# Kernel tuning notes

Measured on AMD Instinct MI355X. Metric: run time of the kernel, lower is better.

## Reference

```python
import jax, jax.numpy as jnp
import numpy as np

N_NODES = 100000

def _gcn_conv(x, W, b, src, dst, ew, num_nodes):
    # x: [N, Fin], W: [Fin, Fout], src/dst: [Etot], ew: [Etot]
    xw = x @ W                                   # [N, Fout]
    deg = jax.ops.segment_sum(ew, dst, num_segments=num_nodes)   # [N]
    dinv = jnp.where(deg > 0, jax.lax.rsqrt(jnp.where(deg > 0, deg, 1.0)), 0.0)
    norm = dinv[src] * ew * dinv[dst]            # [Etot]
    msg = xw[src] * norm[:, None]                # [Etot, Fout] gather-transform
    out = jax.ops.segment_sum(msg, dst, num_segments=num_nodes)  # scatter-add
    return out + b

def setup_inputs() -> dict:
    key = jax.random.key(0)
    k1, k2, k3, k4, k5, k6, k7 = jax.random.split(key, 7)
    N, E, F_IN, HID, CLS = N_NODES, 1600000, 128, 64, 32
    x = jax.random.normal(k1, (N, F_IN), dtype=jnp.float32)
    edge_index = jax.random.randint(k2, (2, E), 0, N, dtype=jnp.int64)
    edge_weight = jax.random.uniform(k3, (E,), dtype=jnp.float32)
    s1 = 1.0 / np.sqrt(F_IN)
    s2 = 1.0 / np.sqrt(HID)
    W1 = jax.random.uniform(k4, (F_IN, HID), dtype=jnp.float32, minval=-s1, maxval=s1)
    b1 = jnp.zeros((HID,), dtype=jnp.float32)
    W2 = jax.random.uniform(k5, (HID, CLS), dtype=jnp.float32, minval=-s2, maxval=s2)
    b2 = jnp.zeros((CLS,), dtype=jnp.float32)
    return {"x": x, "edge_index": edge_index, "edge_weight": edge_weight,
            "W1": W1, "b1": b1, "W2": W2, "b2": b2}

def reference(x, edge_index, edge_weight, W1, b1, W2, b2):
    N = x.shape[0]
    # add self-loops with weight 1 (PyG GCNConv default)
    loop = jnp.arange(N, dtype=edge_index.dtype)
    src = jnp.concatenate([edge_index[0], loop])
    dst = jnp.concatenate([edge_index[1], loop])
    ew = jnp.concatenate([edge_weight, jnp.ones((N,), dtype=edge_weight.dtype)])
    h = _gcn_conv(x, W1, b1, src, dst, ew, N)
    h = jax.nn.relu(h)
    # dropout is identity in eval mode
    out = _gcn_conv(h, W2, b2, src, dst, ew, N)
    return out
```

## Files before the change

### kernel.cpp

```cpp
#include <hip/hip_runtime.h>

#define FIN 128
#define HID 64
#define CLS 32

#define BSH 7
#define BNODES 128
#define GB 256
#define BCAP 4096

__device__ inline unsigned short f2bf(float x) {
  unsigned u = __float_as_uint(x);
  return (unsigned short)((u + 0x7FFFu + ((u >> 16) & 1u)) >> 16);
}
__device__ inline void bf8_to_f32(int4 v, float* f) {
  f[0] = __uint_as_float((unsigned)v.x << 16);
  f[1] = __uint_as_float((unsigned)v.x & 0xFFFF0000u);
  f[2] = __uint_as_float((unsigned)v.y << 16);
  f[3] = __uint_as_float((unsigned)v.y & 0xFFFF0000u);
  f[4] = __uint_as_float((unsigned)v.z << 16);
  f[5] = __uint_as_float((unsigned)v.z & 0xFFFF0000u);
  f[6] = __uint_as_float((unsigned)v.w << 16);
  f[7] = __uint_as_float((unsigned)v.w & 0xFFFF0000u);
}

__global__ __launch_bounds__(256) void k_a1(const int* __restrict__ dst,
                                            int* __restrict__ gcntT,
                                            int E, int CHUNK, int NBUK) {
  __shared__ int cnt[1024];
  for (int i = threadIdx.x; i < NBUK; i += 256) cnt[i] = 0;
  __syncthreads();
  int s = blockIdx.x * CHUNK, e = min(E, s + CHUNK);
  for (int p = s + threadIdx.x; p < e; p += 256)
    atomicAdd(&cnt[dst[p] >> BSH], 1);
  __syncthreads();
  for (int i = threadIdx.x; i < NBUK; i += 256)
    gcntT[i * GB + blockIdx.x] = cnt[i];
}

__global__ __launch_bounds__(256) void k_scan_sums(const int* __restrict__ counts,
                                                   int* __restrict__ bsum, int N) {
  __shared__ int s[256];
  int base = blockIdx.x * 1024 + threadIdx.x * 4;
  int t = 0;
#pragma unroll
  for (int j = 0; j < 4; ++j)
    if (base + j < N) t += counts[base + j];
  s[threadIdx.x] = t;
  __syncthreads();
  for (int off = 128; off > 0; off >>= 1) {
    if (threadIdx.x < off) s[threadIdx.x] += s[threadIdx.x + off];
    __syncthreads();
  }
  if (threadIdx.x == 0) bsum[blockIdx.x] = s[0];
}

__global__ __launch_bounds__(256) void k_scan_bsums(int* __restrict__ bsum, int nb) {
  __shared__ int s[256];
  int t = threadIdx.x;
  int v = (t < nb) ? bsum[t] : 0;
  s[t] = v;
  __syncthreads();
  for (int off = 1; off < 256; off <<= 1) {
    int u = (t >= off) ? s[t - off] : 0;
    __syncthreads();
    s[t] += u;
    __syncthreads();
  }
  if (t < nb) bsum[t] = s[t] - v;
}

__global__ __launch_bounds__(256) void k_scan_emit(const int* __restrict__ counts,
                                                   const int* __restrict__ bsum,
                                                   int* __restrict__ rowstart, int N) {
  __shared__ int s[256];
  int base = blockIdx.x * 1024 + threadIdx.x * 4;
  int c[4];
#pragma unroll
  for (int j = 0; j < 4; ++j) c[j] = (base + j < N) ? counts[base + j] : 0;
  int tsum = c[0] + c[1] + c[2] + c[3];
  s[threadIdx.x] = tsum;
  __syncthreads();
  for (int off = 1; off < 256; off <<= 1) {
    int v = (threadIdx.x >= off) ? s[threadIdx.x - off] : 0;
    __syncthreads();
    s[threadIdx.x] += v;
    __syncthreads();
  }
  int run = bsum[blockIdx.x] + s[threadIdx.x] - tsum;
#pragma unroll
  for (int j = 0; j < 4; ++j) {
    if (base + j < N) rowstart[base + j] = run;
    run += c[j];
  }
}

__global__ __launch_bounds__(256) void k_a2(const int* __restrict__ src,
                                            const int* __restrict__ dst,
                                            const float* __restrict__ ew,
                                            const int* __restrict__ goff,
                                            int2* __restrict__ recs,
                                            int E, int CHUNK, int NBUK) {
  __shared__ int cur[1024];
  for (int i = threadIdx.x; i < NBUK; i += 256)
    cur[i] = goff[i * GB + blockIdx.x];
  __syncthreads();
  int s = blockIdx.x * CHUNK, e = min(E, s + CHUNK);
  for (int p = s + threadIdx.x; p < e; p += 256) {
    int d = dst[p];
    int b = d >> BSH;
    int pos = atomicAdd(&cur[b], 1);
    recs[pos] = make_int2(src[p] | ((d & (BNODES - 1)) << 17), __float_as_int(ew[p]));
  }
}

__global__ __launch_bounds__(256) void k_bucket(int2* __restrict__ recs,
                                                const int* __restrict__ goff,
                                                float* __restrict__ dinv,
                                                int* __restrict__ rowstart,
                                                int N, int E, int NBUK) {
  __shared__ int2 lrec[BCAP];
  __shared__ int cnt[BNODES];
  __shared__ int cur[BNODES];
  __shared__ int sbuf[BNODES];
  __shared__ float degs[BNODES];
  __shared__ float dl[BNODES];
  const int b = blockIdx.x;
  const int t = threadIdx.x;
  const int bstart = goff[b * GB];
  const int bend = (b + 1 < NBUK) ? goff[(b + 1) * GB] : E;
  int m = bend - bstart;
  if (m > BCAP) m = BCAP;

  if (t < BNODES) { cnt[t] = 0; degs[t] = 1.0f; }
  __syncthreads();
  for (int p = t; p < m; p += 256) {
    int2 r = recs[bstart + p];
    lrec[p] = r;
    int d = (r.x >> 17) & (BNODES - 1);
    atomicAdd(&cnt[d], 1);
    atomicAdd(&degs[d], __int_as_float(r.y));
  }
  __syncthreads();
  if (t < BNODES) sbuf[t] = cnt[t];
  __syncthreads();
  for (int off = 1; off < BNODES; off <<= 1) {
    int v = (t < BNODES && t >= off) ? sbuf[t - off] : 0;
    __syncthreads();
    if (t < BNODES) sbuf[t] += v;
    __syncthreads();
  }
  if (t < BNODES) {
    int ls = sbuf[t] - cnt[t];
    cur[t] = ls;
    float di = rsqrtf(degs[t]);
    dl[t] = di;
    int node = b * BNODES + t;
    if (node < N) { dinv[node] = di; rowstart[node] = bstart + ls; }
  }
  __syncthreads();
  for (int p = t; p < m; p += 256) {
    int2 r = lrec[p];
    int d = (r.x >> 17) & (BNODES - 1);
    int pos = atomicAdd(&cur[d], 1);
    float c = __int_as_float(r.y) * dl[d];
    recs[bstart + pos] = make_int2(r.x & 0x1FFFF, __float_as_int(c));
  }
}

template <int K, int F, bool RELU, int BLK, int R, int MINW>
__global__ __launch_bounds__(BLK, MINW) void gemm_kernel(const float* __restrict__ x,
                                                         const float* __restrict__ w,
                                                         const float* __restrict__ scale,
                                                         unsigned short* __restrict__ y, int N) {
  constexpr int CG = F / 4;
  constexpr int RG = BLK / CG;
  constexpr int ROWS = RG * R;
  __shared__ float sW[K * F];
  for (int i = threadIdx.x * 4; i < K * F; i += BLK * 4)
    *(float4*)&sW[i] = *(const float4*)&w[i];
  __syncthreads();

  const int tx = threadIdx.x % CG;
  const int ty = threadIdx.x / CG;
  const int row0 = blockIdx.x * ROWS + ty * R;
  const int col0 = tx * 4;
  if (row0 >= N) return;

  const float* xr[R];
#pragma unroll
  for (int r = 0; r < R; ++r) {
    int rr = (row0 + r < N) ? (row0 + r) : (N - 1);
    xr[r] = x + (size_t)rr * K;
  }

  float acc[R][4] = {{0.f}};
  float4 xv[R], nx[R];
#pragma unroll
  for (int r = 0; r < R; ++r) xv[r] = *(const float4*)&xr[r][0];

  auto step = [&](int k) {
    float4 w0 = *(const float4*)&sW[(k + 0) * F + col0];
    float4 w1 = *(const float4*)&sW[(k + 1) * F + col0];
    float4 w2 = *(const float4*)&sW[(k + 2) * F + col0];
    float4 w3 = *(const float4*)&sW[(k + 3) * F + col0];
#pragma unroll
    for (int r = 0; r < R; ++r) {
      float4 xc = xv[r];
      if (RELU) {
        xc.x = fmaxf(xc.x, 0.f); xc.y = fmaxf(xc.y, 0.f);
        xc.z = fmaxf(xc.z, 0.f); xc.w = fmaxf(xc.w, 0.f);
      }
      acc[r][0] += xc.x * w0.x + xc.y * w1.x + xc.z * w2.x + xc.w * w3.x;
      acc[r][1] += xc.x * w0.y + xc.y * w1.y + xc.z * w2.y + xc.w * w3.y;
      acc[r][2] += xc.x * w0.z + xc.y * w1.z + xc.z * w2.z + xc.w * w3.z;
      acc[r][3] += xc.x * w0.w + xc.y * w1.w + xc.z * w2.w + xc.w * w3.w;
    }
  };

#pragma unroll 4
  for (int k = 0; k < K - 4; k += 4) {
#pragma unroll
    for (int r = 0; r < R; ++r) nx[r] = *(const float4*)&xr[r][k + 4];
    step(k);
#pragma unroll
    for (int r = 0; r < R; ++r) xv[r] = nx[r];
  }
  step(K - 4);

#pragma unroll
  for (int r = 0; r < R; ++r)
    if (row0 + r < N) {
      float sc = scale[row0 + r];
      ushort4 o;
      o.x = f2bf(sc * acc[r][0]); o.y = f2bf(sc * acc[r][1]);
      o.z = f2bf(sc * acc[r][2]); o.w = f2bf(sc * acc[r][3]);
      *(ushort4*)&y[(size_t)(row0 + r) * F + col0] = o;
    }
}

template <int F>
__global__ __launch_bounds__(256) void pull_agg(const unsigned short* __restrict__ xs,
                                                const int2* __restrict__ pairs,
                                                const int* __restrict__ rowstart,
                                                const float* __restrict__ dinv,
                                                const float* __restrict__ b,
                                                float* __restrict__ out, int N, int E) {
  constexpr int LPN = F / 8;
  constexpr int NPB = 256 / LPN;
  const int g = blockIdx.x * NPB + threadIdx.x / LPN;
  const int f8 = (threadIdx.x % LPN) * 8;
  if (g >= N) return;

  const int start = rowstart[g];
  const int end = (g + 1 < N) ? rowstart[g + 1] : E;
  const float di = dinv[g];

  float acc[8];
  {
    int4 v = *(const int4*)&xs[(size_t)g * F + f8];
    float xf[8];
    bf8_to_f32(v, xf);
    float4 b0 = *(const float4*)&b[f8];
    float4 b1 = *(const float4*)&b[f8 + 4];
    acc[0] = fmaf(di, xf[0], b0.x); acc[1] = fmaf(di, xf[1], b0.y);
    acc[2] = fmaf(di, xf[2], b0.z); acc[3] = fmaf(di, xf[3], b0.w);
    acc[4] = fmaf(di, xf[4], b1.x); acc[5] = fmaf(di, xf[5], b1.y);
    acc[6] = fmaf(di, xf[6], b1.z); acc[7] = fmaf(di, xf[7], b1.w);
  }

  int p = start;
  for (; p + 2 <= end; p += 2) {
    int2 p0 = pairs[p];
    int2 p1 = pairs[p + 1];
    int4 v0 = *(const int4*)&xs[(size_t)p0.x * F + f8];
    int4 v1 = *(const int4*)&xs[(size_t)p1.x * F + f8];
    float c0 = __int_as_float(p0.y), c1 = __int_as_float(p1.y);
    float x0[8], x1[8];
    bf8_to_f32(v0, x0);
    bf8_to_f32(v1, x1);
#pragma unroll
    for (int j = 0; j < 8; ++j) acc[j] = fmaf(c0, x0[j], acc[j]);
#pragma unroll
    for (int j = 0; j < 8; ++j) acc[j] = fmaf(c1, x1[j], acc[j]);
  }
  if (p < end) {
    int2 pa = pairs[p];
    int4 va = *(const int4*)&xs[(size_t)pa.x * F + f8];
    float ca = __int_as_float(pa.y);
    float xa[8];
    bf8_to_f32(va, xa);
#pragma unroll
    for (int j = 0; j < 8; ++j) acc[j] = fmaf(ca, xa[j], acc[j]);
  }
  *(float4*)&out[(size_t)g * F + f8] = make_float4(acc[0], acc[1], acc[2], acc[3]);
  *(float4*)&out[(size_t)g * F + f8 + 4] = make_float4(acc[4], acc[5], acc[6], acc[7]);
}

extern "C" void kernel_launch(void* const* d_in, const int* in_sizes, int n_in,
                              void* d_out, int out_size, void* d_ws, size_t ws_size,
                              hipStream_t stream) {
  const float* x  = (const float*)d_in[0];
  const int*   ei = (const int*)d_in[1];
  const float* ew = (const float*)d_in[2];
  const float* W1 = (const float*)d_in[3];
  const float* b1 = (const float*)d_in[4];
  const float* W2 = (const float*)d_in[5];
  const float* b2 = (const float*)d_in[6];
  float* out = (float*)d_out;

  const int N = in_sizes[0] / FIN;
  const int E = in_sizes[2];
  const int* src = ei;
  const int* dst = ei + E;

  const int NBUK = (N + BNODES - 1) >> BSH;
  const int M = NBUK * GB;
  const int CHUNK = (E + GB - 1) / GB;
  const int nbM = (M + 1023) / 1024;

  float* wsf      = (float*)d_ws;
  float* dinv     = wsf;
  int*   rowstart = (int*)(dinv + N);
  int*   gcntT    = rowstart + N;
  int*   bsum     = gcntT + M;
  int2*  recs     = (int2*)(bsum + 256);
  unsigned short* xs1 = (unsigned short*)(recs + E);
  float* out1     = (float*)(xs1 + (size_t)N * HID);
  unsigned short* xs2 = xs1;

  k_a1<<<GB, 256, 0, stream>>>(dst, gcntT, E, CHUNK, NBUK);
  k_scan_sums<<<nbM, 256, 0, stream>>>(gcntT, bsum, M);
  k_scan_bsums<<<1, 256, 0, stream>>>(bsum, nbM);
  k_scan_emit<<<nbM, 256, 0, stream>>>(gcntT, bsum, gcntT, M);
  k_a2<<<GB, 256, 0, stream>>>(src, dst, ew, gcntT, recs, E, CHUNK, NBUK);
  k_bucket<<<NBUK, 256, 0, stream>>>(recs, gcntT, dinv, rowstart, N, E, NBUK);

  gemm_kernel<FIN, HID, false, 256, 4, 6><<<(N + 63) / 64, 256, 0, stream>>>(x, W1, dinv, xs1, N);
  pull_agg<HID><<<(N + 31) / 32, 256, 0, stream>>>(xs1, recs, rowstart, dinv, b1, out1, N, E);

  gemm_kernel<HID, CLS, true, 256, 2, 6><<<(N + 63) / 64, 256, 0, stream>>>(out1, W2, dinv, xs2, N);
  pull_agg<CLS><<<(N + 63) / 64, 256, 0, stream>>>(xs2, recs, rowstart, dinv, b2, out, N, E);
}
```

Measured before the change: 278.7 us.

## Replace scalar FP32 GEMMs with bf16 MFMA kernels using prepacked weights

```diff
diff --git a/kernel.cpp b/kernel.cpp
--- a/kernel.cpp
+++ b/kernel.cpp
@@ -8,6 +8,9 @@
 #define BNODES 128
 #define GB 256
 #define BCAP 4096
+
+using bfrag = __attribute__((ext_vector_type(8))) short;
+using cfrag = __attribute__((ext_vector_type(4))) float;
 
 __device__ inline unsigned short f2bf(float x) {
   unsigned u = __float_as_uint(x);
@@ -22,6 +25,28 @@
   f[5] = __uint_as_float((unsigned)v.z & 0xFFFF0000u);
   f[6] = __uint_as_float((unsigned)v.w << 16);
   f[7] = __uint_as_float((unsigned)v.w & 0xFFFF0000u);
+}
+
+__global__ __launch_bounds__(256) void k_wpack(const float* __restrict__ W1,
+                                               const float* __restrict__ W2,
+                                               unsigned short* __restrict__ wp1,
+                                               unsigned short* __restrict__ wp2) {
+  int t = blockIdx.x * 256 + threadIdx.x;
+  int total = gridDim.x * 256;
+  for (int i = t; i < 16 * 512; i += total) {
+    int f = i >> 9, l = (i >> 3) & 63, j = i & 7;
+    int ks = f >> 2, nt = f & 3;
+    int k = ks * 32 + (l >> 4) * 8 + j;
+    int n = nt * 16 + (l & 15);
+    wp1[i] = f2bf(W1[k * 64 + n]);
+  }
+  for (int i = t; i < 4 * 512; i += total) {
+    int f = i >> 9, l = (i >> 3) & 63, j = i & 7;
+    int ks = f >> 1, nt = f & 1;
+    int k = ks * 32 + (l >> 4) * 8 + j;
+    int n = nt * 16 + (l & 15);
+    wp2[i] = f2bf(W2[k * 32 + n]);
+  }
 }
 
 __global__ __launch_bounds__(256) void k_a1(const int* __restrict__ dst,
@@ -168,74 +193,63 @@
   }
 }
 
-template <int K, int F, bool RELU, int BLK, int R, int MINW>
-__global__ __launch_bounds__(BLK, MINW) void gemm_kernel(const float* __restrict__ x,
-                                                         const float* __restrict__ w,
-                                                         const float* __restrict__ scale,
-                                                         unsigned short* __restrict__ y, int N) {
-  constexpr int CG = F / 4;
-  constexpr int RG = BLK / CG;
-  constexpr int ROWS = RG * R;
-  __shared__ float sW[K * F];
-  for (int i = threadIdx.x * 4; i < K * F; i += BLK * 4)
-    *(float4*)&sW[i] = *(const float4*)&w[i];
-  __syncthreads();
-
-  const int tx = threadIdx.x % CG;
-  const int ty = threadIdx.x / CG;
-  const int row0 = blockIdx.x * ROWS + ty * R;
-  const int col0 = tx * 4;
+template <int K, int F, bool RELU>
+__global__ __launch_bounds__(256, 4) void mfma_gemm(const float* __restrict__ x,
+                                                    const unsigned short* __restrict__ wp,
+                                                    const float* __restrict__ scale,
+                                                    unsigned short* __restrict__ y, int N) {
+  constexpr int KS = K / 32;
+  constexpr int NT = F / 16;
+  const int lane = threadIdx.x & 63;
+  const int quad = lane >> 4;
+  const int col = lane & 15;
+  const int row0 = blockIdx.x * 64 + (threadIdx.x >> 6) * 16;
   if (row0 >= N) return;
 
-  const float* xr[R];
-#pragma unroll
-  for (int r = 0; r < R; ++r) {
-    int rr = (row0 + r < N) ? (row0 + r) : (N - 1);
-    xr[r] = x + (size_t)rr * K;
-  }
-
-  float acc[R][4] = {{0.f}};
-  float4 xv[R], nx[R];
-#pragma unroll
-  for (int r = 0; r < R; ++r) xv[r] = *(const float4*)&xr[r][0];
-
-  auto step = [&](int k) {
-    float4 w0 = *(const float4*)&sW[(k + 0) * F + col0];
-    float4 w1 = *(const float4*)&sW[(k + 1) * F + col0];
-    float4 w2 = *(const float4*)&sW[(k + 2) * F + col0];
-    float4 w3 = *(const float4*)&sW[(k + 3) * F + col0];
-#pragma unroll
-    for (int r = 0; r < R; ++r) {
-      float4 xc = xv[r];
-      if (RELU) {
-        xc.x = fmaxf(xc.x, 0.f); xc.y = fmaxf(xc.y, 0.f);
-        xc.z = fmaxf(xc.z, 0.f); xc.w = fmaxf(xc.w, 0.f);
-      }
-      acc[r][0] += xc.x * w0.x + xc.y * w1.x + xc.z * w2.x + xc.w * w3.x;
-      acc[r][1] += xc.x * w0.y + xc.y * w1.y + xc.z * w2.y + xc.w * w3.y;
-      acc[r][2] += xc.x * w0.z + xc.y * w1.z + xc.z * w2.z + xc.w * w3.z;
-      acc[r][3] += xc.x * w0.w + xc.y * w1.w + xc.z * w2.w + xc.w * w3.w;
+  bfrag bf[KS * NT];
+#pragma unroll
+  for (int f = 0; f < KS * NT; ++f)
+    bf[f] = *(const bfrag*)(wp + f * 512 + lane * 8);
+
+  cfrag acc[NT] = {};
+
+  int row_a = row0 + col;
+  if (row_a >= N) row_a = N - 1;
+  const float* xp = x + (size_t)row_a * K + quad * 8;
+
+#pragma unroll
+  for (int ks = 0; ks < KS; ++ks) {
+    float4 a0 = *(const float4*)(xp + ks * 32);
+    float4 a1 = *(const float4*)(xp + ks * 32 + 4);
+    if (RELU) {
+      a0.x = fmaxf(a0.x, 0.f); a0.y = fmaxf(a0.y, 0.f);
+      a0.z = fmaxf(a0.z, 0.f); a0.w = fmaxf(a0.w, 0.f);
+      a1.x = fmaxf(a1.x, 0.f); a1.y = fmaxf(a1.y, 0.f);
+      a1.z = fmaxf(a1.z, 0.f); a1.w = fmaxf(a1.w, 0.f);
     }
-  };
-
-#pragma unroll 4
-  for (int k = 0; k < K - 4; k += 4) {
-#pragma unroll
-    for (int r = 0; r < R; ++r) nx[r] = *(const float4*)&xr[r][k + 4];
-    step(k);
-#pragma unroll
-    for (int r = 0; r < R; ++r) xv[r] = nx[r];
-  }
-  step(K - 4);
-
-#pragma unroll
-  for (int r = 0; r < R; ++r)
-    if (row0 + r < N) {
-      float sc = scale[row0 + r];
-      ushort4 o;
-      o.x = f2bf(sc * acc[r][0]); o.y = f2bf(sc * acc[r][1]);
-      o.z = f2bf(sc * acc[r][2]); o.w = f2bf(sc * acc[r][3]);
-      *(ushort4*)&y[(size_t)(row0 + r) * F + col0] = o;
+    bfrag af;
+    af[0] = (short)f2bf(a0.x); af[1] = (short)f2bf(a0.y);
+    af[2] = (short)f2bf(a0.z); af[3] = (short)f2bf(a0.w);
+    af[4] = (short)f2bf(a1.x); af[5] = (short)f2bf(a1.y);
+    af[6] = (short)f2bf(a1.z); af[7] = (short)f2bf(a1.w);
+#pragma unroll
+    for (int nt = 0; nt < NT; ++nt)
+      acc[nt] = __builtin_amdgcn_mfma_f32_16x16x32_bf16(af, bf[ks * NT + nt], acc[nt], 0, 0, 0);
+  }
+
+  float scr[4];
+#pragma unroll
+  for (int r = 0; r < 4; ++r) {
+    int row = row0 + quad * 4 + r;
+    scr[r] = (row < N) ? scale[row] : 0.f;
+  }
+#pragma unroll
+  for (int nt = 0; nt < NT; ++nt)
+#pragma unroll
+    for (int r = 0; r < 4; ++r) {
+      int row = row0 + quad * 4 + r;
+      if (row < N)
+        y[(size_t)row * F + nt * 16 + col] = f2bf(scr[r] * acc[nt][r]);
     }
 }
 
@@ -328,7 +342,10 @@
   unsigned short* xs1 = (unsigned short*)(recs + E);
   float* out1     = (float*)(xs1 + (size_t)N * HID);
   unsigned short* xs2 = xs1;
-
+  unsigned short* wp1 = (unsigned short*)(out1 + (size_t)N * HID);
+  unsigned short* wp2 = wp1 + 16 * 512;
+
+  k_wpack<<<32, 256, 0, stream>>>(W1, W2, wp1, wp2);
   k_a1<<<GB, 256, 0, stream>>>(dst, gcntT, E, CHUNK, NBUK);
   k_scan_sums<<<nbM, 256, 0, stream>>>(gcntT, bsum, M);
   k_scan_bsums<<<1, 256, 0, stream>>>(bsum, nbM);
@@ -336,9 +353,9 @@
   k_a2<<<GB, 256, 0, stream>>>(src, dst, ew, gcntT, recs, E, CHUNK, NBUK);
   k_bucket<<<NBUK, 256, 0, stream>>>(recs, gcntT, dinv, rowstart, N, E, NBUK);
 
-  gemm_kernel<FIN, HID, false, 256, 4, 6><<<(N + 63) / 64, 256, 0, stream>>>(x, W1, dinv, xs1, N);
+  mfma_gemm<FIN, HID, false><<<(N + 63) / 64, 256, 0, stream>>>(x, wp1, dinv, xs1, N);
   pull_agg<HID><<<(N + 31) / 32, 256, 0, stream>>>(xs1, recs, rowstart, dinv, b1, out1, N, E);
 
-  gemm_kernel<HID, CLS, true, 256, 2, 6><<<(N + 63) / 64, 256, 0, stream>>>(out1, W2, dinv, xs2, N);
+  mfma_gemm<HID, CLS, true><<<(N + 63) / 64, 256, 0, stream>>>(out1, wp2, dinv, xs2, N);
   pull_agg<CLS><<<(N + 63) / 64, 256, 0, stream>>>(xs2, recs, rowstart, dinv, b2, out, N, E);
 }
```

Result: faster. 254.7 us (-8.6%).
